# Optimization experiments

Hardware: AMD Instinct MI355X
Metric: run time of the kernel (lower is better)

The kernel has to match this reference:

```python
import jax, jax.numpy as jnp
import numpy as np

EPS = 1e-5          # module's self.eps
CLAMP = 1e-8        # numerical floor for norms
MAX_EUCLID = 32.0   # rescale_to_max_euclid cap (best-effort reconstruction)


def _linner(u, v):
    # Lorentz inner product <u,v>_L = -u0*v0 + <u_s,v_s>, keepdims on last axis
    uv = jnp.sum(u * v, axis=-1, keepdims=True)
    return uv - 2.0 * u[..., :1] * v[..., :1]


def _centroid(x):
    # Lorentzian (weighted) centroid: mean then renormalize onto hyperboloid (k=1)
    avg = jnp.mean(x, axis=-2)
    denom = jnp.sqrt(jnp.clip(-_linner(avg, avg), CLAMP, None))
    return avg / denom


def _logmap(x, y):
    # log_x(y) on Lorentz model, k=1
    alpha = jnp.clip(-_linner(x, y), 1.0 + 1e-7, None)
    u = y - alpha * x
    unorm = jnp.sqrt(jnp.clip(_linner(u, u), CLAMP, None))
    return jnp.arccosh(alpha) * u / unorm


def _plus_origin(y):
    # y + o where o = (1, 0, ..., 0)
    return jnp.concatenate([y[..., :1] + 1.0, y[..., 1:]], axis=-1)


def _transp0back(y, v):
    # parallel transport T_{y->o}(v): v + <o,v>_L/(1 - <y,o>_L) * (y + o); <o,v>_L = -v0
    coef = -v[..., :1] / (1.0 + y[..., :1])
    return v + coef * _plus_origin(y)


def _transp0(y, v):
    # parallel transport T_{o->y}(v): v + <y,v>_L/(1 + y0) * (o + y)
    coef = _linner(y, v) / (1.0 + y[..., :1])
    return v + coef * _plus_origin(y)


def _expmap(x, u):
    # exp_x(u) on Lorentz model, k=1
    nu = jnp.sqrt(jnp.clip(_linner(u, u), CLAMP, None))
    return jnp.cosh(nu) * x + jnp.sinh(nu) * u / nu


def _rescale_to_max_euclid(x):
    n = jnp.sqrt(jnp.sum(x * x, axis=-1, keepdims=True))
    return x * jnp.minimum(1.0, MAX_EUCLID / jnp.maximum(n, CLAMP))


def setup_inputs() -> dict:
    key = jax.random.key(0)
    B, S, D = 64, 4096, 128
    raw = 0.5 * jax.random.normal(key, (B, S, D - 1), dtype=jnp.float32)
    time = jnp.sqrt(1.0 + jnp.sum(raw * raw, axis=-1, keepdims=True))
    x = jnp.concatenate([time, raw], axis=-1)  # points on the hyperboloid
    gamma = jnp.ones((D,), dtype=jnp.float32)
    beta = jnp.zeros((D,), dtype=jnp.float32).at[0].set(1.0)  # manifold origin
    return {"x": x, "gamma": gamma, "beta": beta}


def reference(x, gamma, beta):
    # Training-mode Lorentz batchnorm (3D input path)
    mean = _centroid(x)       # (B, D)
    mean = _centroid(mean)    # (D,)
    x_T = _logmap(mean, x)            # tangent vectors at mean, (B, S, D)
    x_T = _transp0back(mean, x_T)     # transport to tangent space at origin
    var = jnp.sqrt(jnp.var(x_T, axis=(0, 1)) + EPS)   # Frechet per-feature std, (D,)
    x_T = x_T * (gamma / (var + EPS))
    x_T = _rescale_to_max_euclid(x_T)
    x_T = _transp0(beta, x_T)         # transport to tangent space at beta
    return _expmap(beta, x_T)
```

## Files before the change

### kernel.cpp

```cpp
#include <hip/hip_runtime.h>
#include <math.h>

#define NB 64
#define NS 4096
#define ND 128
#define NPTS (NB * NS)
#define PPB 256
#define NBLK (NPTS / PPB)
#define EPSV 1e-5f
#define CLAMPV 1e-8f
#define MAXEUC 32.0f

__device__ __forceinline__ float rcp_f(float x) { return __builtin_amdgcn_rcpf(x); }

#define DPP_ADD(v, ctrl)                                                            \
    v += __int_as_float(__builtin_amdgcn_update_dpp(0, __float_as_int(v), (ctrl),   \
                                                    0xF, 0xF, true))

__device__ __forceinline__ float row16_sum(float v) {
    DPP_ADD(v, 0x128);
    DPP_ADD(v, 0x124);
    DPP_ADD(v, 0x122);
    DPP_ADD(v, 0x121);
    return v;
}

__device__ __forceinline__ void point_scalars16(const float4& xa, const float4& xb,
                                                const float4& wa, const float4& wb,
                                                float inv1pm0, int fl,
                                                float& fac, float& hcoef) {
    float ad = wa.x * xa.x + wa.y * xa.y + wa.z * xa.z + wa.w * xa.w
             + wb.x * xb.x + wb.y * xb.y + wb.z * xb.z + wb.w * xb.w;
    float px = (fl == 0) ? xa.x : 0.f;
    ad = row16_sum(ad);
    px = row16_sum(px);
    float alpha = fmaxf(ad, 1.0f + 1e-7f);
    float am1 = alpha * alpha - 1.f;
    float sq = sqrtf(fmaxf(am1, CLAMPV));
    fac = __logf(alpha + sq) * rcp_f(sq);
    hcoef = -fac * (alpha + px) * inv1pm0;
}

__global__ __launch_bounds__(256) void k1(const float4* __restrict__ x4,
                                          float* __restrict__ part1) {
    const int fl = threadIdx.x & 15;
    const int pg = threadIdx.x >> 4;
    const long long base = (long long)blockIdx.x * PPB;
    float4 sa = make_float4(0.f, 0.f, 0.f, 0.f), sb = sa;
#pragma unroll 4
    for (int i = 0; i < PPB / 16; ++i) {
        long long p = base + i * 16 + pg;
        float4 xa = x4[p * 32 + fl];
        float4 xb = x4[p * 32 + fl + 16];
        sa.x += xa.x; sa.y += xa.y; sa.z += xa.z; sa.w += xa.w;
        sb.x += xb.x; sb.y += xb.y; sb.z += xb.z; sb.w += xb.w;
    }
    __shared__ float ls[16][ND];
    float* ps = &ls[pg][fl * 8];
    ps[0] = sa.x; ps[1] = sa.y; ps[2] = sa.z; ps[3] = sa.w;
    ps[4] = sb.x; ps[5] = sb.y; ps[6] = sb.z; ps[7] = sb.w;
    __syncthreads();
    if (threadIdx.x < ND) {
        int d = threadIdx.x;
        int slot = ((d & 63) >> 2) * 8 + (d >> 6) * 4 + (d & 3);
        float S = 0.f;
#pragma unroll
        for (int cc = 0; cc < 16; ++cc) S += ls[cc][slot];
        part1[blockIdx.x * ND + d] = S;
    }
}

__global__ __launch_bounds__(64) void k2a(const float* __restrict__ part1,
                                          float* __restrict__ avg1) {
    const int b = blockIdx.x;
    const int t = threadIdx.x;
    float a0 = 0.f, a1 = 0.f;
#pragma unroll
    for (int c = 0; c < 16; ++c) {
        a0 += part1[(b * 16 + c) * ND + t];
        a1 += part1[(b * 16 + c) * ND + 64 + t];
    }
    a0 *= (1.0f / (float)NS);
    a1 *= (1.0f / (float)NS);
    float s = a0 * a0 + a1 * a1;
#pragma unroll
    for (int o = 32; o > 0; o >>= 1) s += __shfl_xor(s, o, 64);
    float a00 = __shfl(a0, 0, 64);
    float denom = sqrtf(fmaxf(2.f * a00 * a00 - s, CLAMPV));
    avg1[b * ND + t] = a0 / denom;
    avg1[b * ND + 64 + t] = a1 / denom;
}

__global__ __launch_bounds__(64) void k2b(const float* __restrict__ avg1,
                                          float* __restrict__ meanG) {
    const int t = threadIdx.x;
    float a0 = 0.f, a1 = 0.f;
    for (int b = 0; b < NB; ++b) {
        a0 += avg1[b * ND + t];
        a1 += avg1[b * ND + 64 + t];
    }
    a0 *= (1.0f / (float)NB);
    a1 *= (1.0f / (float)NB);
    float s = a0 * a0 + a1 * a1;
#pragma unroll
    for (int o = 32; o > 0; o >>= 1) s += __shfl_xor(s, o, 64);
    float a00 = __shfl(a0, 0, 64);
    float denom = sqrtf(fmaxf(2.f * a00 * a00 - s, CLAMPV));
    meanG[t] = a0 / denom;
    meanG[64 + t] = a1 / denom;
}

__global__ __launch_bounds__(256) void k3(const float4* __restrict__ x4,
                                          const float* __restrict__ meanG,
                                          float* __restrict__ p3S,
                                          float* __restrict__ p3Q,
                                          float2* __restrict__ fchG) {
    const int fl = threadIdx.x & 15;
    const int pg = threadIdx.x >> 4;
    const float4* m4 = (const float4*)meanG;
    const float4 ma = m4[fl], mb = m4[fl + 16];
    const float m0 = meanG[0];
    const float inv1pm0 = rcp_f(1.f + m0);
    float4 wa = make_float4(-ma.x, -ma.y, -ma.z, -ma.w);
    float4 wb = make_float4(-mb.x, -mb.y, -mb.z, -mb.w);
    if (fl == 0) wa.x = ma.x;
    float4 sa = make_float4(0.f, 0.f, 0.f, 0.f), sb = sa, qa = sa, qb = sa;
    const long long base = (long long)blockIdx.x * PPB;
#pragma unroll 4
    for (int i = 0; i < PPB / 16; ++i) {
        long long p = base + i * 16 + pg;
        float4 xa = x4[p * 32 + fl];
        float4 xb = x4[p * 32 + fl + 16];
        float fac, hc;
        point_scalars16(xa, xb, wa, wb, inv1pm0, fl, fac, hc);
        if (fl == 0) fchG[p] = make_float2(fac, hc);
        float t0 = fac * xa.x + hc * ma.x;
        float t1 = fac * xa.y + hc * ma.y;
        float t2 = fac * xa.z + hc * ma.z;
        float t3 = fac * xa.w + hc * ma.w;
        float t4 = fac * xb.x + hc * mb.x;
        float t5 = fac * xb.y + hc * mb.y;
        float t6 = fac * xb.z + hc * mb.z;
        float t7 = fac * xb.w + hc * mb.w;
        if (fl == 0) t0 = 0.f;
        sa.x += t0; sa.y += t1; sa.z += t2; sa.w += t3;
        sb.x += t4; sb.y += t5; sb.z += t6; sb.w += t7;
        qa.x += t0 * t0; qa.y += t1 * t1; qa.z += t2 * t2; qa.w += t3 * t3;
        qb.x += t4 * t4; qb.y += t5 * t5; qb.z += t6 * t6; qb.w += t7 * t7;
    }
    __shared__ float ls[16][ND];
    __shared__ float lq[16][ND];
    float* ps = &ls[pg][fl * 8];
    float* pq = &lq[pg][fl * 8];
    ps[0] = sa.x; ps[1] = sa.y; ps[2] = sa.z; ps[3] = sa.w;
    ps[4] = sb.x; ps[5] = sb.y; ps[6] = sb.z; ps[7] = sb.w;
    pq[0] = qa.x; pq[1] = qa.y; pq[2] = qa.z; pq[3] = qa.w;
    pq[4] = qb.x; pq[5] = qb.y; pq[6] = qb.z; pq[7] = qb.w;
    __syncthreads();
    if (threadIdx.x < ND) {
        int d = threadIdx.x;
        int slot = ((d & 63) >> 2) * 8 + (d >> 6) * 4 + (d & 3);
        float S = 0.f, Q = 0.f;
#pragma unroll
        for (int cc = 0; cc < 16; ++cc) { S += ls[cc][slot]; Q += lq[cc][slot]; }
        p3S[d * NBLK + blockIdx.x] = S;
        p3Q[d * NBLK + blockIdx.x] = Q;
    }
}

__global__ __launch_bounds__(256) void k4(const float* __restrict__ p3S,
                                          const float* __restrict__ p3Q,
                                          const float* __restrict__ gamma,
                                          float* __restrict__ scaleG) {
    const int d = blockIdx.x;
    const int t = threadIdx.x;
    const float4* vS = (const float4*)(p3S + d * NBLK);
    const float4* vQ = (const float4*)(p3Q + d * NBLK);
    float4 a = vS[t];
    float4 b = vQ[t];
    __shared__ double dredS[256];
    __shared__ double dredQ[256];
    dredS[t] = (double)a.x + (double)a.y + (double)a.z + (double)a.w;
    dredQ[t] = (double)b.x + (double)b.y + (double)b.z + (double)b.w;
    __syncthreads();
    for (int o = 128; o > 0; o >>= 1) {
        if (t < o) { dredS[t] += dredS[t + o]; dredQ[t] += dredQ[t + o]; }
        __syncthreads();
    }
    if (t == 0) {
        const double N = (double)NPTS;
        double mu = dredS[0] / N;
        double var = dredQ[0] / N - mu * mu;
        if (var < 0.0) var = 0.0;
        float stdv = sqrtf((float)var + EPSV);
        scaleG[d] = gamma[d] / (stdv + EPSV);
    }
}

__global__ __launch_bounds__(256) void k5(const float4* __restrict__ x4,
                                          const float* __restrict__ meanG,
                                          const float* __restrict__ scaleG,
                                          const float* __restrict__ betaG,
                                          const float2* __restrict__ fchG,
                                          float4* __restrict__ out4) {
    const int fl = threadIdx.x & 15;
    const int pg = threadIdx.x >> 4;
    const float4* m4 = (const float4*)meanG;
    const float4* s4 = (const float4*)scaleG;
    const float4* b4 = (const float4*)betaG;
    const float4 ma = m4[fl], mb = m4[fl + 16];
    const float4 sca = s4[fl], scb = s4[fl + 16];
    const float4 bta = b4[fl], btb = b4[fl + 16];
    const float b0 = betaG[0];
    const float inv1pb0 = rcp_f(1.f + b0);
    const long long base = (long long)blockIdx.x * PPB;
#pragma unroll 4
    for (int i = 0; i < PPB / 16; ++i) {
        long long p = base + i * 16 + pg;
        float4 xa = x4[p * 32 + fl];
        float4 xb = x4[p * 32 + fl + 16];
        float2 fh = fchG[p];
        float fac = fh.x, hc = fh.y;
        float ts0 = sca.x * (fac * xa.x + hc * ma.x);
        float ts1 = sca.y * (fac * xa.y + hc * ma.y);
        float ts2 = sca.z * (fac * xa.z + hc * ma.z);
        float ts3 = sca.w * (fac * xa.w + hc * ma.w);
        float ts4 = scb.x * (fac * xb.x + hc * mb.x);
        float ts5 = scb.y * (fac * xb.y + hc * mb.y);
        float ts6 = scb.z * (fac * xb.z + hc * mb.z);
        float ts7 = scb.w * (fac * xb.w + hc * mb.w);
        if (fl == 0) ts0 = 0.f;
        float nn = ts0 * ts0 + ts1 * ts1 + ts2 * ts2 + ts3 * ts3
                 + ts4 * ts4 + ts5 * ts5 + ts6 * ts6 + ts7 * ts7;
        float bd = bta.x * ts0 + bta.y * ts1 + bta.z * ts2 + bta.w * ts3
                 + btb.x * ts4 + btb.y * ts5 + btb.z * ts6 + btb.w * ts7;
        nn = row16_sum(nn);
        bd = row16_sum(bd);
        float n = sqrtf(nn);
        float r = fminf(1.f, MAXEUC * rcp_f(fmaxf(n, CLAMPV)));
        float coef2 = r * bd * inv1pb0;
        float nu = fmaxf(r * n, 1e-4f);
        float e = __expf(nu);
        float ei = rcp_f(e);
        float ch = 0.5f * (e + ei);
        float sf = (0.5f * (e - ei)) * rcp_f(nu);
        float A = ch + sf * coef2;
        float Bc = sf * r;
        float4 oa, ob;
        oa.x = Bc * ts0 + A * bta.x;
        oa.y = Bc * ts1 + A * bta.y;
        oa.z = Bc * ts2 + A * bta.z;
        oa.w = Bc * ts3 + A * bta.w;
        ob.x = Bc * ts4 + A * btb.x;
        ob.y = Bc * ts5 + A * btb.y;
        ob.z = Bc * ts6 + A * btb.z;
        ob.w = Bc * ts7 + A * btb.w;
        if (fl == 0) oa.x += sf * coef2;
        out4[p * 32 + fl] = oa;
        out4[p * 32 + fl + 16] = ob;
    }
}

extern "C" void kernel_launch(void* const* d_in, const int* in_sizes, int n_in,
                              void* d_out, int out_size, void* d_ws, size_t ws_size,
                              hipStream_t stream) {
    const float* x = (const float*)d_in[0];
    const float* gamma = (const float*)d_in[1];
    const float* beta = (const float*)d_in[2];
    float* out = (float*)d_out;
    float* ws = (float*)d_ws;

    float* part1  = ws;
    float* avg1   = part1 + NBLK * ND;
    float* meanG  = avg1 + NB * ND;
    float* scaleG = meanG + ND;
    float* p3S    = scaleG + ND;
    float* p3Q    = p3S + ND * NBLK;
    float2* fchG  = (float2*)(p3Q + ND * NBLK);

    k1 <<<NBLK, 256, 0, stream>>>((const float4*)x, part1);
    k2a<<<NB, 64, 0, stream>>>(part1, avg1);
    k2b<<<1, 64, 0, stream>>>(avg1, meanG);
    k3 <<<NBLK, 256, 0, stream>>>((const float4*)x, meanG, p3S, p3Q, fchG);
    k4 <<<ND, 256, 0, stream>>>(p3S, p3Q, gamma, scaleG);
    k5 <<<NBLK, 256, 0, stream>>>((const float4*)x, meanG, scaleG, beta, fchG,
                                  (float4*)out);
}
```

Baseline: 287.5 us.

## Streamline centroid reduction, fuse k2 kernels, add nontemporal loads/stores and launch bounds

New measurement: 294.4 us. 1.02x slower.

```diff
diff --git a/kernel.cpp b/kernel.cpp
--- a/kernel.cpp
+++ b/kernel.cpp
@@ -5,11 +5,30 @@
 #define NS 4096
 #define ND 128
 #define NPTS (NB * NS)
+#define PPB1 128
+#define NBLK1 (NPTS / PPB1)
+#define CHUNKS1 (NS / PPB1)
 #define PPB 256
 #define NBLK (NPTS / PPB)
 #define EPSV 1e-5f
 #define CLAMPV 1e-8f
 #define MAXEUC 32.0f
+
+typedef float nfloat4 __attribute__((ext_vector_type(4)));
+typedef float nfloat2 __attribute__((ext_vector_type(2)));
+
+__device__ __forceinline__ float4 nt_load4(const float4* p) {
+    nfloat4 v = __builtin_nontemporal_load((const nfloat4*)p);
+    return make_float4(v.x, v.y, v.z, v.w);
+}
+__device__ __forceinline__ float2 nt_load2(const float2* p) {
+    nfloat2 v = __builtin_nontemporal_load((const nfloat2*)p);
+    return make_float2(v.x, v.y);
+}
+__device__ __forceinline__ void nt_store4(const float4& v, float4* p) {
+    nfloat4 nv = {v.x, v.y, v.z, v.w};
+    __builtin_nontemporal_store(nv, (nfloat4*)p);
+}
 
 __device__ __forceinline__ float rcp_f(float x) { return __builtin_amdgcn_rcpf(x); }
 
@@ -41,80 +60,72 @@
     hcoef = -fac * (alpha + px) * inv1pm0;
 }
 
-__global__ __launch_bounds__(256) void k1(const float4* __restrict__ x4,
-                                          float* __restrict__ part1) {
-    const int fl = threadIdx.x & 15;
-    const int pg = threadIdx.x >> 4;
-    const long long base = (long long)blockIdx.x * PPB;
-    float4 sa = make_float4(0.f, 0.f, 0.f, 0.f), sb = sa;
-#pragma unroll 4
-    for (int i = 0; i < PPB / 16; ++i) {
-        long long p = base + i * 16 + pg;
-        float4 xa = x4[p * 32 + fl];
-        float4 xb = x4[p * 32 + fl + 16];
-        sa.x += xa.x; sa.y += xa.y; sa.z += xa.z; sa.w += xa.w;
-        sb.x += xb.x; sb.y += xb.y; sb.z += xb.z; sb.w += xb.w;
-    }
-    __shared__ float ls[16][ND];
-    float* ps = &ls[pg][fl * 8];
-    ps[0] = sa.x; ps[1] = sa.y; ps[2] = sa.z; ps[3] = sa.w;
-    ps[4] = sb.x; ps[5] = sb.y; ps[6] = sb.z; ps[7] = sb.w;
-    __syncthreads();
-    if (threadIdx.x < ND) {
-        int d = threadIdx.x;
-        int slot = ((d & 63) >> 2) * 8 + (d >> 6) * 4 + (d & 3);
-        float S = 0.f;
-#pragma unroll
-        for (int cc = 0; cc < 16; ++cc) S += ls[cc][slot];
-        part1[blockIdx.x * ND + d] = S;
-    }
-}
-
-__global__ __launch_bounds__(64) void k2a(const float* __restrict__ part1,
-                                          float* __restrict__ avg1) {
-    const int b = blockIdx.x;
-    const int t = threadIdx.x;
-    float a0 = 0.f, a1 = 0.f;
-#pragma unroll
-    for (int c = 0; c < 16; ++c) {
-        a0 += part1[(b * 16 + c) * ND + t];
-        a1 += part1[(b * 16 + c) * ND + 64 + t];
-    }
-    a0 *= (1.0f / (float)NS);
-    a1 *= (1.0f / (float)NS);
-    float s = a0 * a0 + a1 * a1;
-#pragma unroll
-    for (int o = 32; o > 0; o >>= 1) s += __shfl_xor(s, o, 64);
-    float a00 = __shfl(a0, 0, 64);
-    float denom = sqrtf(fmaxf(2.f * a00 * a00 - s, CLAMPV));
-    avg1[b * ND + t] = a0 / denom;
-    avg1[b * ND + 64 + t] = a1 / denom;
-}
-
-__global__ __launch_bounds__(64) void k2b(const float* __restrict__ avg1,
-                                          float* __restrict__ meanG) {
-    const int t = threadIdx.x;
-    float a0 = 0.f, a1 = 0.f;
-    for (int b = 0; b < NB; ++b) {
-        a0 += avg1[b * ND + t];
-        a1 += avg1[b * ND + 64 + t];
-    }
-    a0 *= (1.0f / (float)NB);
-    a1 *= (1.0f / (float)NB);
-    float s = a0 * a0 + a1 * a1;
-#pragma unroll
-    for (int o = 32; o > 0; o >>= 1) s += __shfl_xor(s, o, 64);
-    float a00 = __shfl(a0, 0, 64);
-    float denom = sqrtf(fmaxf(2.f * a00 * a00 - s, CLAMPV));
-    meanG[t] = a0 / denom;
-    meanG[64 + t] = a1 / denom;
-}
-
-__global__ __launch_bounds__(256) void k3(const float4* __restrict__ x4,
-                                          const float* __restrict__ meanG,
-                                          float* __restrict__ p3S,
-                                          float* __restrict__ p3Q,
-                                          float2* __restrict__ fchG) {
+__global__ __launch_bounds__(256, 8) void k1(const float4* __restrict__ x4,
+                                             float4* __restrict__ part1_4) {
+    const int tid = threadIdx.x;
+    const long long base = (long long)blockIdx.x * (PPB1 * 32);
+    float4 acc = make_float4(0.f, 0.f, 0.f, 0.f);
+#pragma unroll 8
+    for (int i = 0; i < PPB1 * 32 / 256; ++i) {
+        float4 v = x4[base + i * 256 + tid];
+        acc.x += v.x; acc.y += v.y; acc.z += v.z; acc.w += v.w;
+    }
+    __shared__ float4 ls4[8][32];
+    ls4[tid >> 5][tid & 31] = acc;
+    __syncthreads();
+    if (tid < 32) {
+        float4 s = ls4[0][tid];
+#pragma unroll
+        for (int c = 1; c < 8; ++c) {
+            float4 v = ls4[c][tid];
+            s.x += v.x; s.y += v.y; s.z += v.z; s.w += v.w;
+        }
+        part1_4[blockIdx.x * 32 + tid] = s;
+    }
+}
+
+__global__ __launch_bounds__(1024) void k2(const float* __restrict__ part1,
+                                           float* __restrict__ meanG) {
+    __shared__ float avgL[NB][ND];
+    const int w = threadIdx.x >> 6, l = threadIdx.x & 63;
+    for (int b = w; b < NB; b += 16) {
+        float a0 = 0.f, a1 = 0.f;
+#pragma unroll
+        for (int c = 0; c < CHUNKS1; ++c) {
+            a0 += part1[(b * CHUNKS1 + c) * ND + l];
+            a1 += part1[(b * CHUNKS1 + c) * ND + 64 + l];
+        }
+        a0 *= (1.0f / (float)NS);
+        a1 *= (1.0f / (float)NS);
+        float s = a0 * a0 + a1 * a1;
+#pragma unroll
+        for (int o = 32; o > 0; o >>= 1) s += __shfl_xor(s, o, 64);
+        float a00 = __shfl(a0, 0, 64);
+        float denom = sqrtf(fmaxf(2.f * a00 * a00 - s, CLAMPV));
+        avgL[b][l] = a0 / denom;
+        avgL[b][64 + l] = a1 / denom;
+    }
+    __syncthreads();
+    if (w == 0) {
+        float a0 = 0.f, a1 = 0.f;
+        for (int b = 0; b < NB; ++b) { a0 += avgL[b][l]; a1 += avgL[b][64 + l]; }
+        a0 *= (1.0f / (float)NB);
+        a1 *= (1.0f / (float)NB);
+        float s = a0 * a0 + a1 * a1;
+#pragma unroll
+        for (int o = 32; o > 0; o >>= 1) s += __shfl_xor(s, o, 64);
+        float a00 = __shfl(a0, 0, 64);
+        float denom = sqrtf(fmaxf(2.f * a00 * a00 - s, CLAMPV));
+        meanG[l] = a0 / denom;
+        meanG[64 + l] = a1 / denom;
+    }
+}
+
+__global__ __launch_bounds__(256, 4) void k3(const float4* __restrict__ x4,
+                                             const float* __restrict__ meanG,
+                                             float* __restrict__ p3S,
+                                             float* __restrict__ p3Q,
+                                             float2* __restrict__ fchG) {
     const int fl = threadIdx.x & 15;
     const int pg = threadIdx.x >> 4;
     const float4* m4 = (const float4*)meanG;
@@ -197,12 +208,12 @@
     }
 }
 
-__global__ __launch_bounds__(256) void k5(const float4* __restrict__ x4,
-                                          const float* __restrict__ meanG,
-                                          const float* __restrict__ scaleG,
-                                          const float* __restrict__ betaG,
-                                          const float2* __restrict__ fchG,
-                                          float4* __restrict__ out4) {
+__global__ __launch_bounds__(256, 4) void k5(const float4* __restrict__ x4,
+                                             const float* __restrict__ meanG,
+                                             const float* __restrict__ scaleG,
+                                             const float* __restrict__ betaG,
+                                             const float2* __restrict__ fchG,
+                                             float4* __restrict__ out4) {
     const int fl = threadIdx.x & 15;
     const int pg = threadIdx.x >> 4;
     const float4* m4 = (const float4*)meanG;
@@ -217,9 +228,9 @@
 #pragma unroll 4
     for (int i = 0; i < PPB / 16; ++i) {
         long long p = base + i * 16 + pg;
-        float4 xa = x4[p * 32 + fl];
-        float4 xb = x4[p * 32 + fl + 16];
-        float2 fh = fchG[p];
+        float4 xa = nt_load4(&x4[p * 32 + fl]);
+        float4 xb = nt_load4(&x4[p * 32 + fl + 16]);
+        float2 fh = nt_load2(&fchG[p]);
         float fac = fh.x, hc = fh.y;
         float ts0 = sca.x * (fac * xa.x + hc * ma.x);
         float ts1 = sca.y * (fac * xa.y + hc * ma.y);
@@ -256,8 +267,8 @@
         ob.z = Bc * ts6 + A * btb.z;
         ob.w = Bc * ts7 + A * btb.w;
         if (fl == 0) oa.x += sf * coef2;
-        out4[p * 32 + fl] = oa;
-        out4[p * 32 + fl + 16] = ob;
+        nt_store4(oa, &out4[p * 32 + fl]);
+        nt_store4(ob, &out4[p * 32 + fl + 16]);
     }
 }
 
@@ -271,18 +282,16 @@
     float* ws = (float*)d_ws;
 
     float* part1  = ws;
-    float* avg1   = part1 + NBLK * ND;
-    float* meanG  = avg1 + NB * ND;
+    float* meanG  = part1 + NBLK1 * ND;
     float* scaleG = meanG + ND;
     float* p3S    = scaleG + ND;
     float* p3Q    = p3S + ND * NBLK;
     float2* fchG  = (float2*)(p3Q + ND * NBLK);
 
-    k1 <<<NBLK, 256, 0, stream>>>((const float4*)x, part1);
-    k2a<<<NB, 64, 0, stream>>>(part1, avg1);
-    k2b<<<1, 64, 0, stream>>>(avg1, meanG);
-    k3 <<<NBLK, 256, 0, stream>>>((const float4*)x, meanG, p3S, p3Q, fchG);
-    k4 <<<ND, 256, 0, stream>>>(p3S, p3Q, gamma, scaleG);
-    k5 <<<NBLK, 256, 0, stream>>>((const float4*)x, meanG, scaleG, beta, fchG,
-                                  (float4*)out);
-}
+    k1<<<NBLK1, 256, 0, stream>>>((const float4*)x, (float4*)part1);
+    k2<<<1, 1024, 0, stream>>>(part1, meanG);
+    k3<<<NBLK, 256, 0, stream>>>((const float4*)x, meanG, p3S, p3Q, fchG);
+    k4<<<ND, 256, 0, stream>>>(p3S, p3Q, gamma, scaleG);
+    k5<<<NBLK, 256, 0, stream>>>((const float4*)x, meanG, scaleG, beta, fchG,
+                                 (float4*)out);
+}
```
